# Optimization experiments

Measured on AMD Instinct MI355X. Metric: run time of the kernel, lower is better.

Reference implementation:

```python
import jax, jax.numpy as jnp
import numpy as np

EMBED_DIM = 1024
NUM_HEADS = 16
HEAD_DIM = EMBED_DIM // NUM_HEADS


def setup_inputs() -> dict:
    key = jax.random.key(0)
    ks = jax.random.split(key, 9)
    B, S, E, hd = 2, 2048, EMBED_DIM, HEAD_DIM
    s_e = 1.0 / np.sqrt(E)
    return {
        "x": jax.random.normal(ks[0], (B, S, E), dtype=jnp.float32),
        "wq": jax.random.uniform(ks[1], (E, E), jnp.float32, -s_e, s_e),
        "bq": jax.random.uniform(ks[2], (E,), jnp.float32, -s_e, s_e),
        "wk": jax.random.uniform(ks[3], (E, hd), jnp.float32, -s_e, s_e),
        "bk": jax.random.uniform(ks[4], (hd,), jnp.float32, -s_e, s_e),
        "wv": jax.random.uniform(ks[5], (E, hd), jnp.float32, -s_e, s_e),
        "bv": jax.random.uniform(ks[6], (hd,), jnp.float32, -s_e, s_e),
        "wo": jax.random.uniform(ks[7], (E, E), jnp.float32, -s_e, s_e),
        "bo": jax.random.uniform(ks[8], (E,), jnp.float32, -s_e, s_e),
    }


def reference(x, wq, bq, wk, bk, wv, bv, wo, bo):
    B, S, E = x.shape
    H, hd = NUM_HEADS, HEAD_DIM
    # projections
    q = (x @ wq + bq).reshape(B, S, H, hd)          # [B,S,H,hd]
    k = x @ wk + bk                                  # [B,S,hd] shared across heads
    v = x @ wv + bv                                  # [B,S,hd]
    scale = 1.0 / np.sqrt(hd).astype(np.float32)
    # scores: [B,H,S_q,S_k]
    scores = jnp.einsum('bqhd,bkd->bhqk', q, k) * scale
    attn = jax.nn.softmax(scores, axis=-1)
    out = jnp.einsum('bhqk,bkd->bqhd', attn, v).reshape(B, S, E)
    return out @ wo + bo
```

## Files before the change

kernel.cpp:

```cpp
#include <hip/hip_runtime.h>
#include <stdint.h>

#define SLEN 2048
#define EDIM 1024
#define NH 16
#define HD 64
#define QLD 1152
#define NSPLIT 4

typedef unsigned short u16;
typedef short bf8 __attribute__((ext_vector_type(8)));
typedef float f4 __attribute__((ext_vector_type(4)));
typedef float f16f __attribute__((ext_vector_type(16)));
typedef int v2i __attribute__((ext_vector_type(2)));
typedef bf8 bf8_a __attribute__((may_alias));
typedef uint2 uint2_a __attribute__((may_alias));
typedef uint4 uint4_a __attribute__((may_alias));

__device__ __forceinline__ float bf2f(u16 u) {
  union { unsigned u; float f; } c; c.u = ((unsigned)u) << 16; return c.f;
}
__device__ __forceinline__ u16 f2bf(float x) {
  union { __bf16 h; u16 u; } c; c.h = (__bf16)x; return c.u;
}
__device__ __forceinline__ unsigned pk2bf(float a, float b) {
  union { __bf16 h[2]; unsigned u; } c;
  c.h[0] = (__bf16)a; c.h[1] = (__bf16)b;
  return c.u;
}
__device__ __forceinline__ void async_cp16(u16* lds, const u16* g) {
  __builtin_amdgcn_global_load_lds((__attribute__((address_space(1))) void*)g,
                                   (__attribute__((address_space(3))) void*)lds,
                                   16, 0, 0);
}

__device__ __forceinline__ void tcvt_tile(const float* src, int srcLd,
                                          u16* dst, int dstLd, int r0, int c0) {
  __shared__ u16 tile[64][65];
  const int t = threadIdx.x;
#pragma unroll
  for (int i = 0; i < 16; ++i) {
    int e = i * 256 + t, rr = e >> 6, cc = e & 63;
    tile[rr][cc] = f2bf(src[(size_t)(r0 + rr) * srcLd + c0 + cc]);
  }
  __syncthreads();
#pragma unroll
  for (int i = 0; i < 16; ++i) {
    int e = i * 256 + t, j = e >> 6, ii = e & 63;
    dst[(size_t)(c0 + j) * dstLd + r0 + ii] = tile[ii][j];
  }
}

__global__ void prep_w(const float* wq, const float* wk, const float* wv,
                       const float* wo, const float* bq, const float* bk,
                       const float* bv, const float* bo, const float* x,
                       u16* wT, u16* woT, float* bQKV, float* bOut, u16* xbf) {
  const int yy = blockIdx.y;
  if (yy < 16) tcvt_tile(wq, 1024, wT, 1024, blockIdx.x * 64, yy * 64);
  else if (yy < 32) tcvt_tile(wo, 1024, woT, 1024, blockIdx.x * 64, (yy - 16) * 64);
  else if (yy == 32) tcvt_tile(wk, 64, wT + (size_t)1024 * 1024, 1024, blockIdx.x * 64, 0);
  else if (yy == 33) tcvt_tile(wv, 64, wT + (size_t)1088 * 1024, 1024, blockIdx.x * 64, 0);
  else if (yy == 34) {
    int i = blockIdx.x * 256 + threadIdx.x;
    if (i < 1024) bQKV[i] = bq[i];
    else if (i < 1088) bQKV[i] = bk[i - 1024];
    else if (i < 1152) bQKV[i] = bv[i - 1088];
    int j = i - 1152;
    if (j >= 0 && j < 1024) bOut[j] = bo[j];
  } else {
    const int blk = (yy - 35) * 16 + blockIdx.x, t = threadIdx.x;
#pragma unroll
    for (int i = 0; i < 8; ++i) {
      int idx = blk * 16384 + i * 2048 + t * 8;
      u16 tmp[8];
#pragma unroll
      for (int j = 0; j < 8; ++j) tmp[j] = f2bf(x[idx + j]);
      *(uint4_a*)&xbf[idx] = *(const uint4_a*)tmp;
    }
  }
}

__global__ __launch_bounds__(256) void gemm_bt_bias(
    const u16* __restrict__ A, const u16* __restrict__ Bt,
    const float* __restrict__ bias, void* __restrict__ C, int K, int ldc,
    int ofp32, u16* __restrict__ vtb) {
  __shared__ __align__(16) u16 As[2][64 * 64];
  __shared__ __align__(16) u16 Bs[2][128 * 64];
  const int tn0 = blockIdx.x * 128, tm0 = blockIdx.y * 64;
  const int tid = threadIdx.x, wave = tid >> 6, lane = tid & 63;
  const int quad = lane >> 4, l16 = lane & 15;
  const int wm = wave & 1, wn = wave >> 1;

  f4 acc[2][4];
#pragma unroll
  for (int i = 0; i < 2; ++i)
#pragma unroll
    for (int j = 0; j < 4; ++j) acc[i][j] = f4{0.f, 0.f, 0.f, 0.f};

  int aslot[2], bslot[4]; size_t aoff[2], boff[4];
#pragma unroll
  for (int i = 0; i < 2; ++i) {
    int s = i * 256 + tid, m = s >> 3, kc = s & 7, c = (kc - m) & 7;
    aslot[i] = s; aoff[i] = (size_t)(tm0 + m) * K + c * 8;
  }
#pragma unroll
  for (int i = 0; i < 4; ++i) {
    int s = i * 256 + tid, n = s >> 3, kc = s & 7, c = (kc - n) & 7;
    bslot[i] = s; boff[i] = (size_t)(tn0 + n) * K + c * 8;
  }
  int ard[2][2], brd[4][2];
#pragma unroll
  for (int mi = 0; mi < 2; ++mi) {
    int m = wm * 32 + mi * 16 + l16;
#pragma unroll
    for (int kk = 0; kk < 2; ++kk)
      ard[mi][kk] = (m * 8 + (((kk * 4 + quad) + m) & 7)) * 8;
  }
#pragma unroll
  for (int ni = 0; ni < 4; ++ni) {
    int n = wn * 64 + ni * 16 + l16;
#pragma unroll
    for (int kk = 0; kk < 2; ++kk)
      brd[ni][kk] = (n * 8 + (((kk * 4 + quad) + n) & 7)) * 8;
  }

  auto stage = [&](int it, int bsel) {
    const size_t kb = (size_t)it * 64;
#pragma unroll
    for (int i = 0; i < 2; ++i)
      async_cp16(&As[bsel][aslot[i] * 8], A + aoff[i] + kb);
#pragma unroll
    for (int i = 0; i < 4; ++i)
      async_cp16(&Bs[bsel][bslot[i] * 8], Bt + boff[i] + kb);
  };

  const int kIt = K >> 6;
  stage(0, 0);
  for (int it = 0; it < kIt; ++it) {
    __syncthreads();
    if (it + 1 < kIt) stage(it + 1, (it + 1) & 1);
    const int bsel = it & 1;
#pragma unroll
    for (int kk = 0; kk < 2; ++kk) {
      bf8 af[2], bfr[4];
#pragma unroll
      for (int mi = 0; mi < 2; ++mi)
        af[mi] = *(const bf8_a*)&As[bsel][ard[mi][kk]];
#pragma unroll
      for (int ni = 0; ni < 4; ++ni)
        bfr[ni] = *(const bf8_a*)&Bs[bsel][brd[ni][kk]];
#pragma unroll
      for (int mi = 0; mi < 2; ++mi)
#pragma unroll
        for (int ni = 0; ni < 4; ++ni)
          acc[mi][ni] = __builtin_amdgcn_mfma_f32_16x16x32_bf16(
              af[mi], bfr[ni], acc[mi][ni], 0, 0, 0);
    }
  }

  float bv[4];
#pragma unroll
  for (int ni = 0; ni < 4; ++ni) bv[ni] = bias[tn0 + wn * 64 + ni * 16 + l16];
#pragma unroll
  for (int mi = 0; mi < 2; ++mi) {
    int row0 = tm0 + wm * 32 + mi * 16 + quad * 4;
#pragma unroll
    for (int ni = 0; ni < 4; ++ni) {
      int col = tn0 + wn * 64 + ni * 16 + l16;
      float vv[4];
#pragma unroll
      for (int r = 0; r < 4; ++r) vv[r] = acc[mi][ni][r] + bv[ni];
      if (ofp32) {
#pragma unroll
        for (int r = 0; r < 4; ++r)
          ((float*)C)[(size_t)(row0 + r) * ldc + col] = vv[r];
      } else {
#pragma unroll
        for (int r = 0; r < 4; ++r)
          ((u16*)C)[(size_t)(row0 + r) * ldc + col] = f2bf(vv[r]);
      }
      if (vtb != nullptr && col >= 1088) {
        int d = col - 1088, bb = row0 >> 11, s0 = row0 & 2047;
        uint2 pk;
        pk.x = pk2bf(vv[0], vv[1]);
        pk.y = pk2bf(vv[2], vv[3]);
        *(uint2_a*)&vtb[(size_t)(bb * 64 + d) * SLEN + s0] = pk;
      }
    }
  }
}

__global__ __launch_bounds__(256, 5) void attn_kernel(
    const u16* __restrict__ qkv, const u16* __restrict__ vT,
    u16* __restrict__ Opart, float* __restrict__ lpart) {
  __shared__ __align__(16) u16 Kf[2][4096];
  __shared__ __align__(16) u16 Vf[2][4096];
  const int qt = blockIdx.x, bh = blockIdx.y, ks = blockIdx.z;
  const int b = bh >> 4, h = bh & 15;
  const int tid = threadIdx.x, wave = tid >> 6, lane = tid & 63;
  const int l31 = lane & 31, hi = lane >> 5, r16l = lane & 15;
  const int base_k = (l31 >> 4) * 64 + hi * 16 + r16l;

  u16* Kflat = &Kf[0][0];
#pragma unroll
  for (int i = 0; i < 4; ++i) {
    int d = i * 256 + tid;
    int kk = d >> 9, g = (d >> 6) & 7, qd = (d >> 4) & 3, r16 = d & 15;
    async_cp16(&Kflat[d * 8],
               qkv + (size_t)(b * SLEN + qt * 128 + g * 16 + r16) * QLD +
                   h * HD + (kk * 4 + qd) * 8);
  }
  __syncthreads();
  bf8 bq[4];
#pragma unroll
  for (int kk2 = 0; kk2 < 4; ++kk2) {
    int c = base_k + wave * 128 + (kk2 >> 1) * 512 + (kk2 & 1) * 32;
    bq[kk2] = *(const bf8_a*)&Kflat[c * 8];
  }
  __syncthreads();

  const int kbase = ks * (SLEN / NSPLIT);
  auto stage = [&](int hh, int bsel) {
#pragma unroll
    for (int i = 0; i < 2; ++i) {
      int d = i * 256 + tid;
      int kk = d >> 8, k8 = (d >> 6) & 3, qd = (d >> 4) & 3, r16 = d & 15;
      async_cp16(&Kf[bsel][d * 8],
                 qkv + (size_t)(b * SLEN + kbase + hh * 64 + k8 * 16 + r16) * QLD +
                     EDIM + (kk * 4 + qd) * 8);
    }
#pragma unroll
    for (int i = 0; i < 2; ++i) {
      int d = i * 256 + tid;
      int k4 = d >> 8, ni = (d >> 6) & 3, qd = (d >> 4) & 3, r16 = d & 15;
      async_cp16(&Vf[bsel][d * 8],
                 vT + (size_t)(b * 64 + ni * 16 + r16) * SLEN + kbase + hh * 64 +
                     (k4 * 4 + qd) * 8);
    }
  };
  stage(0, 0);

  f16f acc_o[2];
#pragma unroll
  for (int i = 0; i < 2; ++i)
#pragma unroll
    for (int r = 0; r < 16; ++r) acc_o[i][r] = 0.f;
  float lr = 0.f;
  const float C1 = 0.125f * 1.44269504089f;

  const int NHALF = SLEN / NSPLIT / 64;
  for (int hh = 0; hh < NHALF; ++hh) {
    __syncthreads();
    if (hh < NHALF - 1) stage(hh + 1, (hh + 1) & 1);
    const int bsel = hh & 1;
    const u16* kf = &Kf[bsel][0];
    const u16* vf = &Vf[bsel][0];

#pragma unroll
    for (int j32 = 0; j32 < 2; ++j32) {
      f16f st;
#pragma unroll
      for (int r = 0; r < 16; ++r) st[r] = 0.f;
      __builtin_amdgcn_s_setprio(1);
#pragma unroll
      for (int kk2 = 0; kk2 < 4; ++kk2) {
        bf8 ak = *(const bf8_a*)
            &kf[(base_k + (kk2 >> 1) * 256 + j32 * 128 + (kk2 & 1) * 32) * 8];
        st = __builtin_amdgcn_mfma_f32_32x32x16_bf16(ak, bq[kk2], st, 0, 0, 0);
      }
      __builtin_amdgcn_s_setprio(0);

      float pe[16];
#pragma unroll
      for (int r = 0; r < 16; ++r) {
        pe[r] = __builtin_amdgcn_exp2f(st[r] * C1);
        lr += pe[r];
      }
      int a0 = (int)pk2bf(pe[0], pe[1]),   b0 = (int)pk2bf(pe[4], pe[5]);
      int a1 = (int)pk2bf(pe[2], pe[3]),   b1 = (int)pk2bf(pe[6], pe[7]);
      int a2 = (int)pk2bf(pe[8], pe[9]),   b2 = (int)pk2bf(pe[12], pe[13]);
      int a3 = (int)pk2bf(pe[10], pe[11]), b3 = (int)pk2bf(pe[14], pe[15]);
      v2i s0 = __builtin_amdgcn_permlane32_swap(a0, b0, false, false);
      v2i s1 = __builtin_amdgcn_permlane32_swap(a1, b1, false, false);
      v2i s2 = __builtin_amdgcn_permlane32_swap(a2, b2, false, false);
      v2i s3 = __builtin_amdgcn_permlane32_swap(a3, b3, false, false);
      union { int i[4]; bf8 v; } up0, up1;
      up0.i[0] = s0[0]; up0.i[1] = s1[0]; up0.i[2] = s0[1]; up0.i[3] = s1[1];
      up1.i[0] = s2[0]; up1.i[1] = s3[0]; up1.i[2] = s2[1]; up1.i[3] = s3[1];

      __builtin_amdgcn_s_setprio(1);
#pragma unroll
      for (int ks2 = 0; ks2 < 2; ++ks2) {
        bf8 pa = ks2 ? up1.v : up0.v;
#pragma unroll
        for (int ni2 = 0; ni2 < 2; ++ni2) {
          bf8 bv = *(const bf8_a*)
              &vf[(base_k + j32 * 256 + ni2 * 128 + ks2 * 32) * 8];
          acc_o[ni2] = __builtin_amdgcn_mfma_f32_32x32x16_bf16(
              pa, bv, acc_o[ni2], 0, 0, 0);
        }
      }
      __builtin_amdgcn_s_setprio(0);
    }
  }

  const size_t pbase = (size_t)((ks * 32 + bh) * 16 + qt) * 128;
  float s = lr + __shfl_xor(lr, 32, 64);
  if (lane < 32) lpart[pbase + wave * 32 + lane] = s;
#pragma unroll
  for (int ni2 = 0; ni2 < 2; ++ni2)
#pragma unroll
    for (int r = 0; r < 16; ++r) {
      int q = (r & 3) + 8 * (r >> 2) + 4 * hi;
      Opart[(pbase + wave * 32 + q) * 64 + ni2 * 32 + l31] =
          f2bf(acc_o[ni2][r]);
    }
}

__global__ __launch_bounds__(256) void reduce_o(const u16* __restrict__ Op,
                                                const float* __restrict__ lp,
                                                u16* __restrict__ aob) {
  const int qt = blockIdx.x, bh = blockIdx.y, b = bh >> 4, h = bh & 15;
  const int t = threadIdx.x, r = t >> 1, dh = (t & 1) * 32;
  size_t p[NSPLIT];
#pragma unroll
  for (int i = 0; i < NSPLIT; ++i)
    p[i] = (size_t)((i * 32 + bh) * 16 + qt) * 128;
  float lsum = 0.f;
#pragma unroll
  for (int i = 0; i < NSPLIT; ++i) lsum += lp[p[i] + r];
  const float inv = 1.f / lsum;
  u16* dst = aob + (size_t)(b * SLEN + qt * 128 + r) * EDIM + h * HD + dh;
#pragma unroll
  for (int c = 0; c < 4; ++c) {
    float accv[8] = {0.f, 0.f, 0.f, 0.f, 0.f, 0.f, 0.f, 0.f};
#pragma unroll
    for (int i = 0; i < NSPLIT; ++i) {
      uint4 a = *(const uint4_a*)(Op + (p[i] + r) * 64 + dh + c * 8);
      const u16* pa = (const u16*)&a;
#pragma unroll
      for (int j = 0; j < 8; ++j) accv[j] += bf2f(pa[j]);
    }
    u16 outv[8];
#pragma unroll
    for (int j = 0; j < 8; ++j) outv[j] = f2bf(accv[j] * inv);
    *(uint4_a*)(dst + c * 8) = *(const uint4_a*)outv;
  }
}

extern "C" void kernel_launch(void* const* d_in, const int* in_sizes, int n_in,
                              void* d_out, int out_size, void* d_ws, size_t ws_size,
                              hipStream_t stream) {
  const float* x  = (const float*)d_in[0];
  const float* wq = (const float*)d_in[1];
  const float* bq = (const float*)d_in[2];
  const float* wk = (const float*)d_in[3];
  const float* bk = (const float*)d_in[4];
  const float* wv = (const float*)d_in[5];
  const float* bv = (const float*)d_in[6];
  const float* wo = (const float*)d_in[7];
  const float* bo = (const float*)d_in[8];

  char* ws = (char*)d_ws;
  size_t off = 0;
  auto carve = [&](size_t bytes) {
    void* p = ws + off;
    off = (off + bytes + 255) & ~(size_t)255;
    return p;
  };
  u16* wT      = (u16*)carve((size_t)1152 * 1024 * 2);
  u16* woT     = (u16*)carve((size_t)1024 * 1024 * 2);
  float* bQKV  = (float*)carve(1152 * 4);
  float* bOut  = (float*)carve(1024 * 4);
  u16* xbf     = (u16*)carve((size_t)4096 * EDIM * 2);
  u16* qkvb    = (u16*)carve((size_t)4096 * QLD * 2);
  u16* vTb     = (u16*)carve((size_t)2 * 64 * SLEN * 2);
  u16* Opart   = (u16*)carve((size_t)NSPLIT * 32 * 16 * 128 * 64 * 2);
  float* lpart = (float*)carve((size_t)NSPLIT * 32 * 16 * 128 * 4);
  u16* aob     = (u16*)carve((size_t)4096 * EDIM * 2);

  prep_w<<<dim3(16, 51), 256, 0, stream>>>(wq, wk, wv, wo, bq, bk, bv, bo, x,
                                           wT, woT, bQKV, bOut, xbf);

  gemm_bt_bias<<<dim3(9, 64), 256, 0, stream>>>(xbf, wT, bQKV, qkvb, 1024, QLD,
                                                0, vTb);

  attn_kernel<<<dim3(16, 32, NSPLIT), 256, 0, stream>>>(qkvb, vTb, Opart, lpart);
  reduce_o<<<dim3(16, 32), 256, 0, stream>>>(Opart, lpart, aob);

  gemm_bt_bias<<<dim3(8, 64), 256, 0, stream>>>(aob, woT, bOut, d_out, 1024,
                                                1024, 1, nullptr);
}
```

Measured before the change: 189.5 us.

## Fold softmax scale into Q projection, halve attention key split, single-buffer GEMM

Several changes at once. The Q columns of the QKV projection epilogue are multiplied by the softmax scale and log2(e), so the attention kernel applies exp2 directly to raw scores. Row sums are kept in four partial accumulators to shorten the dependency chain. Attention staging pointers are precomputed and advanced by increments. NSPLIT drops from 4 to 2 and the attention occupancy hint from 5 to 4 blocks, giving fewer, longer blocks and less reduction work. The GEMM goes from double-buffered async loads to a single buffer with two barriers per K step, which removes load/compute overlap in exchange for less shared memory.

```diff
diff --git a/kernel.cpp b/kernel.cpp
--- a/kernel.cpp
+++ b/kernel.cpp
@@ -6,7 +6,7 @@
 #define NH 16
 #define HD 64
 #define QLD 1152
-#define NSPLIT 4
+#define NSPLIT 2
 
 typedef unsigned short u16;
 typedef short bf8 __attribute__((ext_vector_type(8)));
@@ -84,8 +84,8 @@
     const u16* __restrict__ A, const u16* __restrict__ Bt,
     const float* __restrict__ bias, void* __restrict__ C, int K, int ldc,
     int ofp32, u16* __restrict__ vtb) {
-  __shared__ __align__(16) u16 As[2][64 * 64];
-  __shared__ __align__(16) u16 Bs[2][128 * 64];
+  __shared__ __align__(16) u16 As[64 * 64];
+  __shared__ __align__(16) u16 Bs[128 * 64];
   const int tn0 = blockIdx.x * 128, tm0 = blockIdx.y * 64;
   const int tid = threadIdx.x, wave = tid >> 6, lane = tid & 63;
   const int quad = lane >> 4, l16 = lane & 15;
@@ -124,31 +124,22 @@
       brd[ni][kk] = (n * 8 + (((kk * 4 + quad) + n) & 7)) * 8;
   }
 
-  auto stage = [&](int it, int bsel) {
-    const size_t kb = (size_t)it * 64;
-#pragma unroll
-    for (int i = 0; i < 2; ++i)
-      async_cp16(&As[bsel][aslot[i] * 8], A + aoff[i] + kb);
-#pragma unroll
-    for (int i = 0; i < 4; ++i)
-      async_cp16(&Bs[bsel][bslot[i] * 8], Bt + boff[i] + kb);
-  };
-
   const int kIt = K >> 6;
-  stage(0, 0);
   for (int it = 0; it < kIt; ++it) {
     __syncthreads();
-    if (it + 1 < kIt) stage(it + 1, (it + 1) & 1);
-    const int bsel = it & 1;
+    const size_t kb = (size_t)it * 64;
+#pragma unroll
+    for (int i = 0; i < 2; ++i) async_cp16(&As[aslot[i] * 8], A + aoff[i] + kb);
+#pragma unroll
+    for (int i = 0; i < 4; ++i) async_cp16(&Bs[bslot[i] * 8], Bt + boff[i] + kb);
+    __syncthreads();
 #pragma unroll
     for (int kk = 0; kk < 2; ++kk) {
       bf8 af[2], bfr[4];
 #pragma unroll
-      for (int mi = 0; mi < 2; ++mi)
-        af[mi] = *(const bf8_a*)&As[bsel][ard[mi][kk]];
-#pragma unroll
-      for (int ni = 0; ni < 4; ++ni)
-        bfr[ni] = *(const bf8_a*)&Bs[bsel][brd[ni][kk]];
+      for (int mi = 0; mi < 2; ++mi) af[mi] = *(const bf8_a*)&As[ard[mi][kk]];
+#pragma unroll
+      for (int ni = 0; ni < 4; ++ni) bfr[ni] = *(const bf8_a*)&Bs[brd[ni][kk]];
 #pragma unroll
       for (int mi = 0; mi < 2; ++mi)
 #pragma unroll
@@ -158,6 +149,7 @@
     }
   }
 
+  const float QSCALE = 0.125f * 1.44269504089f;
   float bv[4];
 #pragma unroll
   for (int ni = 0; ni < 4; ++ni) bv[ni] = bias[tn0 + wn * 64 + ni * 16 + l16];
@@ -170,6 +162,10 @@
       float vv[4];
 #pragma unroll
       for (int r = 0; r < 4; ++r) vv[r] = acc[mi][ni][r] + bv[ni];
+      if (vtb != nullptr && col < 1024) {
+#pragma unroll
+        for (int r = 0; r < 4; ++r) vv[r] *= QSCALE;
+      }
       if (ofp32) {
 #pragma unroll
         for (int r = 0; r < 4; ++r)
@@ -190,7 +186,7 @@
   }
 }
 
-__global__ __launch_bounds__(256, 5) void attn_kernel(
+__global__ __launch_bounds__(256, 4) void attn_kernel(
     const u16* __restrict__ qkv, const u16* __restrict__ vT,
     u16* __restrict__ Opart, float* __restrict__ lpart) {
   __shared__ __align__(16) u16 Kf[2][4096];
@@ -220,38 +216,40 @@
   __syncthreads();
 
   const int kbase = ks * (SLEN / NSPLIT);
-  auto stage = [&](int hh, int bsel) {
+  const u16* kp[2]; const u16* vp[2];
+#pragma unroll
+  for (int i = 0; i < 2; ++i) {
+    int d = i * 256 + tid;
+    int kk = d >> 8, k8 = (d >> 6) & 3, qd = (d >> 4) & 3, r16 = d & 15;
+    kp[i] = qkv + (size_t)(b * SLEN + kbase + k8 * 16 + r16) * QLD + EDIM +
+            (kk * 4 + qd) * 8;
+    int k4 = d >> 8, ni = (d >> 6) & 3;
+    vp[i] = vT + (size_t)(b * 64 + ni * 16 + r16) * SLEN + kbase +
+            (k4 * 4 + qd) * 8;
+  }
+  auto stage = [&](int bsel) {
 #pragma unroll
     for (int i = 0; i < 2; ++i) {
       int d = i * 256 + tid;
-      int kk = d >> 8, k8 = (d >> 6) & 3, qd = (d >> 4) & 3, r16 = d & 15;
-      async_cp16(&Kf[bsel][d * 8],
-                 qkv + (size_t)(b * SLEN + kbase + hh * 64 + k8 * 16 + r16) * QLD +
-                     EDIM + (kk * 4 + qd) * 8);
-    }
-#pragma unroll
-    for (int i = 0; i < 2; ++i) {
-      int d = i * 256 + tid;
-      int k4 = d >> 8, ni = (d >> 6) & 3, qd = (d >> 4) & 3, r16 = d & 15;
-      async_cp16(&Vf[bsel][d * 8],
-                 vT + (size_t)(b * 64 + ni * 16 + r16) * SLEN + kbase + hh * 64 +
-                     (k4 * 4 + qd) * 8);
+      async_cp16(&Kf[bsel][d * 8], kp[i]);
+      async_cp16(&Vf[bsel][d * 8], vp[i]);
+      kp[i] += 64 * QLD;
+      vp[i] += 64;
     }
   };
-  stage(0, 0);
+  stage(0);
 
   f16f acc_o[2];
 #pragma unroll
   for (int i = 0; i < 2; ++i)
 #pragma unroll
     for (int r = 0; r < 16; ++r) acc_o[i][r] = 0.f;
-  float lr = 0.f;
-  const float C1 = 0.125f * 1.44269504089f;
+  f4 lracc = f4{0.f, 0.f, 0.f, 0.f};
 
   const int NHALF = SLEN / NSPLIT / 64;
   for (int hh = 0; hh < NHALF; ++hh) {
     __syncthreads();
-    if (hh < NHALF - 1) stage(hh + 1, (hh + 1) & 1);
+    if (hh < NHALF - 1) stage((hh + 1) & 1);
     const int bsel = hh & 1;
     const u16* kf = &Kf[bsel][0];
     const u16* vf = &Vf[bsel][0];
@@ -273,8 +271,8 @@
       float pe[16];
 #pragma unroll
       for (int r = 0; r < 16; ++r) {
-        pe[r] = __builtin_amdgcn_exp2f(st[r] * C1);
-        lr += pe[r];
+        pe[r] = __builtin_amdgcn_exp2f(st[r]);
+        lracc[r & 3] += pe[r];
       }
       int a0 = (int)pk2bf(pe[0], pe[1]),   b0 = (int)pk2bf(pe[4], pe[5]);
       int a1 = (int)pk2bf(pe[2], pe[3]),   b1 = (int)pk2bf(pe[6], pe[7]);
@@ -305,6 +303,7 @@
   }
 
   const size_t pbase = (size_t)((ks * 32 + bh) * 16 + qt) * 128;
+  float lr = (lracc[0] + lracc[1]) + (lracc[2] + lracc[3]);
   float s = lr + __shfl_xor(lr, 32, 64);
   if (lane < 32) lpart[pbase + wave * 32 + lane] = s;
 #pragma unroll
```

Result: faster. 181.1 us (-4.5%).
